# Kernel optimization log

Hardware: AMD Instinct MI355X
Metric: run time of the kernel (lower is better)

The kernel has to match this reference:

```python
import jax, jax.numpy as jnp
import numpy as np

K_KDE = 64
K_RIPS = 16
SCALE = 20.0
DESTNUM = 5
SQRT2 = 1.4142135623730951


def _knn(x, k):
    # squared-euclidean kNN (self included), mirrors FAISS IndexFlatL2 search
    sq = jnp.sum(x * x, axis=1)
    d2 = jnp.maximum(sq[:, None] + sq[None, :] - 2.0 * (x @ x.T), 0.0)
    neg_d, idx = jax.lax.top_k(-d2, k)
    return -neg_d, idx


def _density_map(x, k, scale):
    # KDE density: sum of RBF kernels over k nearest neighbours, max-normalized
    d2, idx = _knn(x, k)
    dens = jnp.sum(jnp.exp(-d2 / scale), axis=1) / (k * scale)
    return dens / jnp.max(dens), idx


def _cluster_pairs(density_sorted, rips_idxs):
    # ToMATo-style union-find over points in decreasing density order.
    # density_sorted is ascending, so index == density rank (inherently
    # sequential on host, as in the original torch module).
    N = density_sorted.shape[0]
    root = np.arange(N)

    def find(i):
        while root[i] != i:
            root[i] = root[root[i]]
            i = root[i]
        return i

    pairs = []
    for i in range(N - 2, -1, -1):
        us = rips_idxs[i][rips_idxs[i] > i]  # upper star: higher-density nbrs
        if us.size == 0:
            continue  # local maximum: births a new cluster
        root[i] = find(int(us.max()))
        for j in us:
            rj, ri = find(int(j)), find(i)
            if rj != ri:
                lo, hi = (ri, rj) if ri < rj else (rj, ri)
                if density_sorted[lo] - density_sorted[i] < 1.0:  # threshold=1
                    root[lo] = hi
                    pairs.append((lo, i))
    see = np.array(pairs, dtype=np.int64)
    # per birth peak, keep the earliest (highest-density) death index
    pd = []
    for b in np.unique(see[:, 0]):
        pd.append([b, see[see[:, 0] == b, 1].max()])
    return np.array(pd, dtype=np.int64)


def setup_inputs() -> dict:
    key = jax.random.key(0)
    x = jax.random.normal(key, (4096, 16), dtype=jnp.float32)
    return {"x": x}


def reference(x):
    kde_dists, kde_idxs = _density_map(x, K_KDE, SCALE)
    sorted_idxs = jnp.argsort(kde_dists)                 # ascending density
    kde_dists_s = kde_dists[sorted_idxs]
    inv_perm = jnp.argsort(sorted_idxs)                  # inverse permutation
    kde_idxs_s = inv_perm[kde_idxs[sorted_idxs]]         # newI1 remap
    pc = x[sorted_idxs]
    _, rips_idxs = _knn(pc, K_RIPS)                      # Rips graph on sorted pc
    pd_pairs = jnp.asarray(
        _cluster_pairs(
            np.asarray(jax.device_get(kde_dists_s)),
            np.asarray(jax.device_get(rips_idxs)),
        )
    )  # [M, 2] (birth_idx, death_idx)
    oripd = kde_dists_s[pd_pairs]                        # [M, 2] densities
    order = jnp.argsort(oripd[:, 0] - oripd[:, 1])       # by persistence, asc
    changepairs = pd_pairs[order[:-DESTNUM]]             # pairs to kill
    nochangepairs = pd_pairs[order[-DESTNUM:-1]]         # pairs to keep
    dest = oripd[order[-1]]                              # most persistent pair
    pd11 = kde_dists_s[changepairs]
    weakdist = jnp.sum(pd11[:, 0] - pd11[:, 1]) / SQRT2
    strongdist = jnp.sum(jnp.linalg.norm(kde_dists_s[nochangepairs] - dest, axis=1))
    return weakdist + strongdist, rips_idxs
```

## Files before the change

kernel.cpp:

```cpp
#include <hip/hip_runtime.h>

#define NPTS 4096
#define DIM 16
#define KKDE 64
#define KRIPS 16
#define CANDCAP 512

typedef unsigned long long u64;
typedef unsigned int u32;
typedef unsigned short u16;

__device__ inline float xla_expf_fma(float input) {
  float x = fminf(input, 88.3762626647950f);
  x = fmaxf(x, -88.3762626647949f);
  float fx = floorf(__builtin_fmaf(x, 1.44269504088896341f, 0.5f));
  x = __builtin_fmaf(fx, -0.693359375f, x);
  x = __builtin_fmaf(fx, 2.12194440e-4f, x);
  float z = __fmul_rn(x, x);
  float y = __builtin_fmaf(x, 1.9875691500e-4f, 1.3981999507e-3f);
  y = __builtin_fmaf(y, x, 8.3334519073e-3f);
  y = __builtin_fmaf(y, x, 4.1665795894e-2f);
  y = __builtin_fmaf(y, x, 1.6666665459e-1f);
  y = __builtin_fmaf(y, x, 5.0000001201e-1f);
  y = __builtin_fmaf(y, z, x);
  y = __fadd_rn(1.0f, y);
  int n = (int)fx;
  float p2n = __uint_as_float(((u32)(n + 127)) << 23);
  return fmaxf(__fmul_rn(y, p2n), input);
}

__device__ inline float llvm_tree16(const float* a) {
  float b[8], c[4], d[2];
#pragma unroll
  for (int j = 0; j < 8; j++) b[j] = __fadd_rn(a[j], a[j + 8]);
#pragma unroll
  for (int j = 0; j < 4; j++) c[j] = __fadd_rn(b[j], b[j + 4]);
  d[0] = __fadd_rn(c[0], c[2]);
  d[1] = __fadd_rn(c[1], c[3]);
  return __fadd_rn(d[0], d[1]);
}

__global__ void sq_kernel(const float* __restrict__ x, float* __restrict__ sq) {
  int i = blockIdx.x * blockDim.x + threadIdx.x;
  if (i >= NPTS) return;
  const float4* xp = (const float4*)(x + i * DIM);
  float4 a0 = xp[0], a1 = xp[1], a2 = xp[2], a3 = xp[3];
  float v[16] = {a0.x, a0.y, a0.z, a0.w, a1.x, a1.y, a1.z, a1.w,
                 a2.x, a2.y, a2.z, a2.w, a3.x, a3.y, a3.z, a3.w};
  float p[16];
#pragma unroll
  for (int d = 0; d < 16; d++) p[d] = __fmul_rn(v[d], v[d]);
  sq[i] = llvm_tree16(p);
}

__device__ inline float d2_formula(float sqi, float sqj, float acc) {
  float d2 = __builtin_fmaf(-2.0f, acc, __fadd_rn(sqi, sqj));
  return fmaxf(d2, 0.0f);
}

__global__ __launch_bounds__(256) void dens_kernel(const float* __restrict__ x,
                                                   const float* __restrict__ sq,
                                                   float* __restrict__ dens,
                                                   u16* __restrict__ knnj) {
  __shared__ u32 hist[4096];
  __shared__ u32 csum[256];
  __shared__ u64 cand[CANDCAP];
  __shared__ float e_sh[KKDE];
  __shared__ float xish[DIM];
  __shared__ float sqish;
  __shared__ int sh_chunkB, sh_baseChunk, sh_B, sh_cnt;
  const int i = blockIdx.x;
  const int tid = threadIdx.x;
  for (int h = tid; h < 4096; h += 256) hist[h] = 0u;
  if (tid < DIM) xish[tid] = x[i * DIM + tid];
  if (tid == 0) { sqish = sq[i]; sh_cnt = 0; }
  __syncthreads();
  float xi[16];
#pragma unroll
  for (int d = 0; d < 16; d++) xi[d] = xish[d];
  const float sqi = sqish;
  u64 keys[16];
#pragma unroll
  for (int s = 0; s < NPTS / 256; s++) {
    int j = tid + 256 * s;
    const float4* xp = (const float4*)(x + j * DIM);
    float4 b0 = xp[0], b1 = xp[1], b2 = xp[2], b3 = xp[3];
    float xj[16] = {b0.x, b0.y, b0.z, b0.w, b1.x, b1.y, b1.z, b1.w,
                    b2.x, b2.y, b2.z, b2.w, b3.x, b3.y, b3.z, b3.w};
    float acc = 0.f;
#pragma unroll
    for (int d = 0; d < 16; d++) acc = __builtin_fmaf(xi[d], xj[d], acc);
    float d2 = d2_formula(sqi, sq[j], acc);
    u64 key = (((u64)__float_as_uint(d2)) << 32) | (u32)j;
    keys[s] = key;
    atomicAdd(&hist[(u32)(key >> 52)], 1u);
  }
  __syncthreads();
  u32 cs = 0;
#pragma unroll
  for (int b2 = 0; b2 < 16; b2++) cs += hist[tid * 16 + b2];
  csum[tid] = cs;
  __syncthreads();
  for (int off = 1; off < 256; off <<= 1) {
    u32 v = csum[tid];
    u32 add = (tid >= off) ? csum[tid - off] : 0u;
    __syncthreads();
    csum[tid] = v + add;
    __syncthreads();
  }
  if (csum[tid] >= KKDE && (tid == 0 || csum[tid - 1] < KKDE)) {
    sh_chunkB = tid;
    sh_baseChunk = (tid == 0) ? 0 : (int)csum[tid - 1];
  }
  __syncthreads();
  if (tid < 16) {
    int h = (int)hist[sh_chunkB * 16 + tid];
    int cum = h;
#pragma unroll
    for (int off = 1; off < 16; off <<= 1) {
      int o = __shfl_up(cum, off, 16);
      if (tid >= off) cum += o;
    }
    int prev = cum - h;
    if (sh_baseChunk + cum >= KKDE && sh_baseChunk + prev < KKDE)
      sh_B = sh_chunkB * 16 + tid;
  }
  __syncthreads();
  const u32 B = (u32)sh_B;
#pragma unroll
  for (int s = 0; s < NPTS / 256; s++) {
    if ((u32)(keys[s] >> 52) <= B) {
      int pos = atomicAdd(&sh_cnt, 1);
      if (pos < CANDCAP) cand[pos] = keys[s];
    }
  }
  __syncthreads();
  const int cnt = (sh_cnt < CANDCAP) ? sh_cnt : CANDCAP;
  for (int c = tid; c < cnt; c += 256) {
    u64 mykey = cand[c];
    int rank = 0;
    for (int t = 0; t < cnt; t++) rank += (cand[t] < mykey) ? 1 : 0;
    if (rank < KKDE) {
      knnj[i * KKDE + rank] = (u16)(mykey & 0xFFFFull);
      float d2v = __uint_as_float((u32)(mykey >> 32));
      e_sh[rank] = xla_expf_fma(__fmul_rn(-d2v, 0.05f));
    }
  }
  __syncthreads();
  if (tid == 0) {
    float lane[16];
#pragma unroll
    for (int j = 0; j < 16; j++) lane[j] = e_sh[j];
#pragma unroll
    for (int k = 1; k < 4; k++)
#pragma unroll
      for (int j = 0; j < 16; j++)
        lane[j] = __fadd_rn(lane[j], e_sh[16 * k + j]);
    float s = llvm_tree16(lane);
    dens[i] = __fmul_rn(s, (1.0f / 1280.0f));
  }
}

__device__ inline void bitonicM(u64* k, int tid, int M) {
  for (int ksz = 2; ksz <= M; ksz <<= 1) {
    for (int jsz = ksz >> 1; jsz > 0; jsz >>= 1) {
      __syncthreads();
      for (int idx = tid; idx < M; idx += 1024) {
        int ixj = idx ^ jsz;
        if (ixj > idx) {
          bool up = ((idx & ksz) == 0);
          u64 a = k[idx], b = k[ixj];
          if ((a > b) == up) { k[idx] = b; k[ixj] = a; }
        }
      }
    }
  }
  __syncthreads();
}

__global__ __launch_bounds__(1024) void sort_kernel(const float* __restrict__ dens,
                                                    int* __restrict__ sidx,
                                                    float* __restrict__ dens_s,
                                                    int* __restrict__ invp) {
  __shared__ u64 k[NPTS];
  __shared__ float red[1024];
  int tid = threadIdx.x;
  float m = 0.0f;
  for (int i = tid; i < NPTS; i += 1024) m = fmaxf(m, dens[i]);
  red[tid] = m;
  __syncthreads();
  for (int off = 512; off > 0; off >>= 1) {
    if (tid < off) red[tid] = fmaxf(red[tid], red[tid + off]);
    __syncthreads();
  }
  float mx = red[0];
  for (int i = tid; i < NPTS; i += 1024) {
    float dn = __fdiv_rn(dens[i], mx);
    k[i] = (((u64)__float_as_uint(dn)) << 32) | (u32)i;
  }
  bitonicM(k, tid, NPTS);
  for (int i = tid; i < NPTS; i += 1024) {
    u64 key = k[i];
    int si = (int)(key & 0xffffffffull);
    sidx[i] = si;
    invp[si] = i;
    dens_s[i] = __uint_as_float((u32)(key >> 32));
  }
}

__global__ __launch_bounds__(64) void rips_kernel(const float* __restrict__ x,
                                                  const float* __restrict__ sq,
                                                  const int* __restrict__ sidx,
                                                  const int* __restrict__ invp,
                                                  const u16* __restrict__ knnj,
                                                  u16* __restrict__ rips,
                                                  int* __restrict__ maxu,
                                                  float* __restrict__ outIdx) {
  const int p = blockIdx.x;
  const int lane = threadIdx.x;
  const int s0 = sidx[p];
  const float sqi = sq[s0];
  float xi[16];
  const float4* xip = (const float4*)(x + s0 * DIM);
  float4 i0 = xip[0], i1 = xip[1], i2 = xip[2], i3 = xip[3];
  xi[0] = i0.x; xi[1] = i0.y; xi[2] = i0.z; xi[3] = i0.w;
  xi[4] = i1.x; xi[5] = i1.y; xi[6] = i1.z; xi[7] = i1.w;
  xi[8] = i2.x; xi[9] = i2.y; xi[10] = i2.z; xi[11] = i2.w;
  xi[12] = i3.x; xi[13] = i3.y; xi[14] = i3.z; xi[15] = i3.w;
  int j = (int)knnj[s0 * KKDE + lane];
  const float4* xp = (const float4*)(x + j * DIM);
  float4 b0 = xp[0], b1 = xp[1], b2 = xp[2], b3 = xp[3];
  float xj[16] = {b0.x, b0.y, b0.z, b0.w, b1.x, b1.y, b1.z, b1.w,
                  b2.x, b2.y, b2.z, b2.w, b3.x, b3.y, b3.z, b3.w};
  float acc = 0.f;
#pragma unroll
  for (int d = 0; d < 16; d++) acc = __builtin_fmaf(xi[d], xj[d], acc);
  float d2 = d2_formula(sqi, sq[j], acc);
  int q = invp[j];
  u64 key = (((u64)__float_as_uint(d2)) << 32) | (u32)q;
#pragma unroll
  for (int ksz = 2; ksz <= 64; ksz <<= 1) {
#pragma unroll
    for (int jm = 32; jm > 0; jm >>= 1) {
      if (jm < ksz) {
        u64 partner = __shfl_xor(key, jm);
        bool up = ((lane & ksz) == 0);
        bool low = ((lane & jm) == 0);
        u64 mn = (partner < key) ? partner : key;
        u64 mx = (partner < key) ? key : partner;
        key = (low == up) ? mn : mx;
      }
    }
  }
  int wj = (int)(key & 0xffffffffull);
  if (lane < KRIPS) {
    rips[p * KRIPS + lane] = (u16)wj;
    outIdx[p * KRIPS + lane] = (float)wj;
  }
  int mu = (lane < KRIPS && wj > p) ? wj : -1;
#pragma unroll
  for (int off = 32; off > 0; off >>= 1) {
    int o = __shfl_xor(mu, off);
    mu = (o > mu) ? o : mu;
  }
  if (lane == 0) maxu[p] = mu;
}

__device__ inline int uf_find(int* root, int v) {
  while (true) {
    int p = root[v];
    if (p == v) return v;
    int g = root[p];
    if (g == p) return p;
    root[v] = g;
    v = g;
  }
}

__global__ __launch_bounds__(1024) void uf_kernel(const u16* __restrict__ rips,
                                                  const int* __restrict__ maxu,
                                                  int* __restrict__ pairs,
                                                  int* __restrict__ paircnt) {
  __shared__ int root[NPTS];
  __shared__ int death[NPTS];
  __shared__ u32 jr[4096];
  __shared__ int elist[256];
  __shared__ u32 mask[8];
  __shared__ int scanb[1024];
  const int tid = threadIdx.x;
  const int slot = tid & 15;
  for (int v = tid; v < NPTS; v += 1024) {
    int m = maxu[v];
    root[v] = (m >= 0) ? m : v;
    death[v] = -1;
  }
  if (tid < 8) mask[tid] = 0u;
  __syncthreads();
  for (int it = 0; it < 13; it++) {
    for (int v = tid; v < NPTS; v += 1024) root[v] = root[root[v]];
    __syncthreads();
  }
  for (int b = (NPTS / 256) - 1; b >= 0; b--) {
#pragma unroll
    for (int p = 0; p < 4; p++) {
      int ii_local = p * 64 + (tid >> 4);
      int ii = b * 256 + ii_local;
      int jj = -1;
      if (ii <= NPTS - 2) {
        int t = (int)rips[ii * KRIPS + slot];
        if (t > ii) jj = t;
      }
      int r = (jj >= 0) ? uf_find(root, jj) : -1;
      jr[ii_local * 16 + slot] = (jj >= 0) ? (u32)r : ~0u;
      const int wg = (tid & 63) >> 4;
      u64 vb = __ballot(jj >= 0);
      u32 vs = (u32)((vb >> (wg * 16)) & 0xFFFFull);
      int fl = wg * 16 + (vs ? (__ffs(vs) - 1) : 0);
      int fv = __shfl(r, fl);
      u64 db = __ballot(jj >= 0 && r != fv);
      bool flagged = (vs != 0u) && (((db >> (wg * 16)) & 0xFFFFull) != 0ull);
      if (slot == 0 && flagged)
        atomicOr(&mask[ii_local >> 5], 1u << (ii_local & 31));
    }
    __syncthreads();
    if (tid < 64) {
      const int lane = tid;
      const int g = lane >> 4;
      const int sl = lane & 15;
      int ne = 0;
      {
        int cnt = 0;
#pragma unroll
        for (int w = 7; w >= 0; w--) cnt += __popc(mask[w]);
        ne = cnt;
      }
      for (int base2 = 0; base2 < ne; base2 += 64) {
        int k2 = base2 + lane;
        if (k2 < ne) {
          int cnt = 0, ev2 = -1;
#pragma unroll
          for (int w = 7; w >= 0; w--) {
            u32 mwv = mask[w];
            int c = __popc(mwv);
            if (ev2 < 0 && k2 < cnt + c) {
              int need = k2 - cnt;
              u32 m = mwv;
              for (int t2 = 0; t2 < need; t2++) m &= ~(1u << (31 - __clz(m)));
              ev2 = w * 32 + (31 - __clz(m));
            }
            cnt += c;
          }
          elist[k2] = ev2;
        }
      }
      asm volatile("s_waitcnt lgkmcnt(0)" ::: "memory");
      int e_nx = (g < ne) ? elist[g] : -1;
      u32 jrw_nx = (e_nx >= 0) ? jr[e_nx * 16 + sl] : ~0u;
      for (int k4 = 0; k4 < ne; k4 += 4) {
        const int e = e_nx;
        const u32 jrw = jrw_nx;
        {
          int idx2 = k4 + 4 + g;
          e_nx = (idx2 < ne) ? elist[idx2] : -1;
          jrw_nx = (e_nx >= 0) ? jr[e_nx * 16 + sl] : ~0u;
        }
        const bool act = (jrw != ~0u);
        int rr0 = act ? (int)jrw : 0;
        int pv = root[rr0];
        int rr = -1;
        if (act) rr = (pv == rr0) ? rr0 : uf_find(root, rr0);
        int t = act ? rr : -1;
#pragma unroll
        for (int off = 8; off > 0; off >>= 1) {
          int o = __shfl_xor(t, off, 16);
          t = (o > t) ? o : t;
        }
        int mx = t;
        const int ev = (e >= 0) ? (b * 256 + e) : -1;
#pragma unroll
        for (int gg = 0; gg < 4; gg++) {
          u64 kb = __ballot(act && rr != mx);
          u32 kg = (u32)((kb >> (gg * 16)) & 0xFFFFull);
          while (kg) {
            int tl = gg * 16 + (__ffs(kg) - 1);
            kg &= kg - 1;
            int kr = __shfl(rr, tl);
            int mxg = __shfl(mx, tl);
            if (kr != mxg) {
              int ig = __shfl(ev, tl);
              if (lane == 0) { root[kr] = mxg; death[kr] = ig; }
              bool hit = act && (rr == kr);
              u64 hb = __ballot(hit);
              if (hit) rr = mxg;
              if ((hb >> (g * 16)) & 0xFFFFull) mx = (mxg > mx) ? mxg : mx;
            }
          }
        }
      }
      if (lane < 8) mask[lane] = 0u;
    }
    __syncthreads();
  }
  int base = tid * 4;
  int l0 = death[base + 0], l1 = death[base + 1];
  int l2 = death[base + 2], l3 = death[base + 3];
  int c = (l0 >= 0) + (l1 >= 0) + (l2 >= 0) + (l3 >= 0);
  scanb[tid] = c;
  __syncthreads();
  for (int off = 1; off < 1024; off <<= 1) {
    int add = (tid >= off) ? scanb[tid - off] : 0;
    __syncthreads();
    scanb[tid] += add;
    __syncthreads();
  }
  int pos = scanb[tid] - c;
  if (l0 >= 0) { pairs[2 * pos] = base + 0; pairs[2 * pos + 1] = l0; pos++; }
  if (l1 >= 0) { pairs[2 * pos] = base + 1; pairs[2 * pos + 1] = l1; pos++; }
  if (l2 >= 0) { pairs[2 * pos] = base + 2; pairs[2 * pos + 1] = l2; pos++; }
  if (l3 >= 0) { pairs[2 * pos] = base + 3; pairs[2 * pos + 1] = l3; pos++; }
  if (tid == 1023) paircnt[0] = scanb[1023];
}

__global__ __launch_bounds__(1024) void final_kernel(const int* __restrict__ pairs,
                                                     const int* __restrict__ paircnt,
                                                     const float* __restrict__ dens_s,
                                                     int* __restrict__ pdb,
                                                     int* __restrict__ pdd,
                                                     float* __restrict__ out0) {
  __shared__ u64 k[NPTS];
  __shared__ double red[1024];
  const int tid = threadIdx.x;
  const int P = paircnt[0];
  int M = 256;
  while (M < P) M <<= 1;
  for (int i = tid; i < P; i += 1024) {
    pdb[i] = pairs[2 * i];
    pdd[i] = pairs[2 * i + 1];
  }
  for (int i = tid; i < M; i += 1024) {
    u64 key = ~0ull;
    if (i < P) {
      float pe = __fsub_rn(dens_s[pairs[2 * i]], dens_s[pairs[2 * i + 1]]);
      key = (((u64)__float_as_uint(pe)) << 32) | (u32)i;
    }
    k[i] = key;
  }
  bitonicM(k, tid, M);
  double a = 0.0;
  const int lim = P - 5;
  for (int rnk = tid; rnk < lim; rnk += 1024) {
    int pp = (int)(k[rnk] & 0xffffffffull);
    a += (double)(dens_s[pdb[pp]] - dens_s[pdd[pp]]);
  }
  red[tid] = a;
  __syncthreads();
  for (int off = 512; off > 0; off >>= 1) {
    if (tid < off) red[tid] += red[tid + off];
    __syncthreads();
  }
  if (tid == 0 && P > 0) {
    double weakdist = red[0] / 1.4142135623730951;
    int plast = (int)(k[P - 1] & 0xffffffffull);
    float dest0 = dens_s[pdb[plast]];
    float dest1 = dens_s[pdd[plast]];
    double strong = 0.0;
    for (int rnk = P - 5; rnk <= P - 2; rnk++) {
      if (rnk < 0) continue;
      int pp = (int)(k[rnk] & 0xffffffffull);
      double dx = (double)dens_s[pdb[pp]] - (double)dest0;
      double dy = (double)dens_s[pdd[pp]] - (double)dest1;
      strong += sqrt(dx * dx + dy * dy);
    }
    out0[0] = (float)(weakdist + strong);
  }
}

extern "C" void kernel_launch(void* const* d_in, const int* in_sizes, int n_in,
                              void* d_out, int out_size, void* d_ws, size_t ws_size,
                              hipStream_t stream) {
  const float* x = (const float*)d_in[0];
  float* out = (float*)d_out;
  char* ws = (char*)d_ws;
  size_t off = 0;
  float* sq = (float*)(ws + off);     off += NPTS * 4;
  float* dens = (float*)(ws + off);   off += NPTS * 4;
  float* dens_s = (float*)(ws + off); off += NPTS * 4;
  int* sidx = (int*)(ws + off);       off += NPTS * 4;
  int* invp = (int*)(ws + off);       off += NPTS * 4;
  int* maxu = (int*)(ws + off);       off += NPTS * 4;
  u16* rips = (u16*)(ws + off);       off += NPTS * KRIPS * 2;
  int* pairs = (int*)(ws + off);      off += NPTS * 2 * 4;
  int* paircnt = (int*)(ws + off);    off += 256;
  int* pdb = (int*)(ws + off);        off += NPTS * 4;
  int* pdd = (int*)(ws + off);        off += NPTS * 4;
  u16* knnj = (u16*)(ws + off);       off += NPTS * KKDE * 2;

  sq_kernel<<<dim3(NPTS / 256), dim3(256), 0, stream>>>(x, sq);
  dens_kernel<<<dim3(NPTS), dim3(256), 0, stream>>>(x, sq, dens, knnj);
  sort_kernel<<<dim3(1), dim3(1024), 0, stream>>>(dens, sidx, dens_s, invp);
  rips_kernel<<<dim3(NPTS), dim3(64), 0, stream>>>(x, sq, sidx, invp, knnj,
                                                   rips, maxu, out + 1);
  uf_kernel<<<dim3(1), dim3(1024), 0, stream>>>(rips, maxu, pairs, paircnt);
  final_kernel<<<dim3(1), dim3(1024), 0, stream>>>(pairs, paircnt, dens_s, pdb, pdd, out);
}
```

Measured before the change: 266.7 us.

## Overlap next batch's root finds with sequential union phase via double buffering

Software-pipelines the union-find kernel. While wavefront 0 runs the sequential merge for the current 256-point batch, the other 15 wavefronts already compute root lookups and conflict masks for the next batch into a second jr/mask buffer. This removes the separate find phase and one barrier per batch from the critical path. The cost is that lookups read root concurrently with merges, so roots may be stale. This relies on union-only monotonicity and the later re-find to stay correct.

```diff
diff --git a/kernel.cpp b/kernel.cpp
--- a/kernel.cpp
+++ b/kernel.cpp
@@ -283,46 +283,55 @@
                                                   int* __restrict__ paircnt) {
   __shared__ int root[NPTS];
   __shared__ int death[NPTS];
-  __shared__ u32 jr[4096];
+  __shared__ u32 jr[2][4096];
   __shared__ int elist[256];
-  __shared__ u32 mask[8];
+  __shared__ u32 mask[2][8];
   __shared__ int scanb[1024];
   const int tid = threadIdx.x;
-  const int slot = tid & 15;
   for (int v = tid; v < NPTS; v += 1024) {
     int m = maxu[v];
     root[v] = (m >= 0) ? m : v;
     death[v] = -1;
   }
-  if (tid < 8) mask[tid] = 0u;
+  if (tid < 16) mask[tid >> 3][tid & 7] = 0u;
   __syncthreads();
   for (int it = 0; it < 13; it++) {
     for (int v = tid; v < NPTS; v += 1024) root[v] = root[root[v]];
     __syncthreads();
   }
+
+#define FIND_BATCH(bb, q)                                                     \
+  {                                                                           \
+    const int slot = tid & 15;                                                \
+    const int grp = (tid - 64) >> 4;                               \
+    const int wg = (tid & 63) >> 4;                                           \
+    _Pragma("unroll")                                                         \
+    for (int pass = 0; pass < 5; pass++) {                                    \
+      int ii_local = pass * 60 + grp;                                         \
+      bool vev = (ii_local < 256);                                            \
+      int ii = (bb) * 256 + ii_local;                                         \
+      int jj = -1;                                                            \
+      if (vev && ii <= NPTS - 2) {                                            \
+        int t = (int)rips[ii * KRIPS + slot];                                 \
+        if (t > ii) jj = t;                                                   \
+      }                                                                       \
+      int r = (jj >= 0) ? uf_find(root, jj) : -1;                             \
+      if (vev) jr[q][ii_local * 16 + slot] = (jj >= 0) ? (u32)r : ~0u;        \
+      u64 vb = __ballot(jj >= 0);                                             \
+      u32 vs = (u32)((vb >> (wg * 16)) & 0xFFFFull);                          \
+      int fl = wg * 16 + (vs ? (__ffs(vs) - 1) : 0);                          \
+      int fv = __shfl(r, fl);                                                 \
+      u64 db = __ballot(jj >= 0 && r != fv);                                  \
+      bool flagged = (vs != 0u) && (((db >> (wg * 16)) & 0xFFFFull) != 0ull); \
+      if (vev && slot == 0 && flagged)                                        \
+        atomicOr(&mask[q][ii_local >> 5], 1u << (ii_local & 31));             \
+    }                                                                         \
+  }
+
+  if (tid >= 64) FIND_BATCH(15, 0);
+  __syncthreads();
+  int cur = 0;
   for (int b = (NPTS / 256) - 1; b >= 0; b--) {
-#pragma unroll
-    for (int p = 0; p < 4; p++) {
-      int ii_local = p * 64 + (tid >> 4);
-      int ii = b * 256 + ii_local;
-      int jj = -1;
-      if (ii <= NPTS - 2) {
-        int t = (int)rips[ii * KRIPS + slot];
-        if (t > ii) jj = t;
-      }
-      int r = (jj >= 0) ? uf_find(root, jj) : -1;
-      jr[ii_local * 16 + slot] = (jj >= 0) ? (u32)r : ~0u;
-      const int wg = (tid & 63) >> 4;
-      u64 vb = __ballot(jj >= 0);
-      u32 vs = (u32)((vb >> (wg * 16)) & 0xFFFFull);
-      int fl = wg * 16 + (vs ? (__ffs(vs) - 1) : 0);
-      int fv = __shfl(r, fl);
-      u64 db = __ballot(jj >= 0 && r != fv);
-      bool flagged = (vs != 0u) && (((db >> (wg * 16)) & 0xFFFFull) != 0ull);
-      if (slot == 0 && flagged)
-        atomicOr(&mask[ii_local >> 5], 1u << (ii_local & 31));
-    }
-    __syncthreads();
     if (tid < 64) {
       const int lane = tid;
       const int g = lane >> 4;
@@ -331,7 +340,7 @@
       {
         int cnt = 0;
 #pragma unroll
-        for (int w = 7; w >= 0; w--) cnt += __popc(mask[w]);
+        for (int w = 7; w >= 0; w--) cnt += __popc(mask[cur][w]);
         ne = cnt;
       }
       for (int base2 = 0; base2 < ne; base2 += 64) {
@@ -340,7 +349,7 @@
           int cnt = 0, ev2 = -1;
 #pragma unroll
           for (int w = 7; w >= 0; w--) {
-            u32 mwv = mask[w];
+            u32 mwv = mask[cur][w];
             int c = __popc(mwv);
             if (ev2 < 0 && k2 < cnt + c) {
               int need = k2 - cnt;
@@ -355,14 +364,14 @@
       }
       asm volatile("s_waitcnt lgkmcnt(0)" ::: "memory");
       int e_nx = (g < ne) ? elist[g] : -1;
-      u32 jrw_nx = (e_nx >= 0) ? jr[e_nx * 16 + sl] : ~0u;
+      u32 jrw_nx = (e_nx >= 0) ? jr[cur][e_nx * 16 + sl] : ~0u;
       for (int k4 = 0; k4 < ne; k4 += 4) {
         const int e = e_nx;
         const u32 jrw = jrw_nx;
         {
           int idx2 = k4 + 4 + g;
           e_nx = (idx2 < ne) ? elist[idx2] : -1;
-          jrw_nx = (e_nx >= 0) ? jr[e_nx * 16 + sl] : ~0u;
+          jrw_nx = (e_nx >= 0) ? jr[cur][e_nx * 16 + sl] : ~0u;
         }
         const bool act = (jrw != ~0u);
         int rr0 = act ? (int)jrw : 0;
@@ -397,10 +406,14 @@
           }
         }
       }
-      if (lane < 8) mask[lane] = 0u;
-    }
-    __syncthreads();
-  }
+      if (lane < 8) mask[cur][lane] = 0u;
+    } else if (b > 0) {
+      FIND_BATCH(b - 1, cur ^ 1);
+    }
+    __syncthreads();
+    cur ^= 1;
+  }
+#undef FIND_BATCH
   int base = tid * 4;
   int l0 = death[base + 0], l1 = death[base + 1];
   int l2 = death[base + 2], l3 = death[base + 3];
```

After: 301.1 us. 1.13x slower.
